# Performance work log

Hardware: AMD Instinct MI355X
Metric: run time of the kernel (lower is better)

Reference implementation:

```python
import jax, jax.numpy as jnp
import numpy as np

B, N, D, P, V = 8, 256, 300, 128, 50001  # batch, seq len, emb dim, proj dim, vocab(+unk)


def setup_inputs() -> dict:
    key = jax.random.key(0)
    ks = jax.random.split(key, 10)
    s = 1.0 / np.sqrt(D)
    sp = 1.0 / np.sqrt(P)
    emb = jax.random.normal(ks[0], (V, D), jnp.float32)
    emb = emb.at[-1].set(0.0)  # unk row zeroed, matches add_unk
    return {
        "sentence": jax.random.randint(ks[1], (B, N), 0, V),
        "emb": emb,
        "Wl": jax.random.uniform(ks[2], (P, D), jnp.float32, -s, s),
        "bl": jnp.zeros((P,), jnp.float32),
        "Wr": jax.random.uniform(ks[3], (P, D), jnp.float32, -s, s),
        "Wo": jax.random.uniform(ks[4], (1, P), jnp.float32, -sp, sp),
        "bo": jnp.zeros((1,), jnp.float32),
        "Ws1": jax.random.uniform(ks[5], (P, D), jnp.float32, -s, s),
        "bs1": jnp.zeros((P,), jnp.float32),
        "Ws2": jax.random.uniform(ks[6], (1, P), jnp.float32, -sp, sp),
        "bs2": jnp.zeros((1,), jnp.float32),
        "We1": jax.random.uniform(ks[7], (P, D), jnp.float32, -s, s),
        "be1": jnp.zeros((P,), jnp.float32),
        "We2": jax.random.uniform(ks[8], (1, P), jnp.float32, -sp, sp),
        "be2": jnp.zeros((1,), jnp.float32),
    }


def reference(sentence, emb, Wl, bl, Wr, Wo, bo, Ws1, bs1, Ws2, bs2, We1, be1, We2, be2):
    x = emb[sentence]                                   # [B,N,D] embedding lookup
    start = jax.nn.relu(x @ Ws1.T + bs1) @ Ws2.T + bs2  # [B,N,1]
    end = jax.nn.relu(x @ We1.T + be1) @ We2.T + be2    # [B,N,1]
    left = x @ Wl.T + bl                                # [B,N,P]
    right = x @ Wr.T                                    # [B,N,P]
    # proj[b,i,j,p] = left[b,j,p] + right[b,i,p]  (unsqueeze(1) + unsqueeze(2))
    proj = left[:, None, :, :] + right[:, :, None, :]   # [B,N,N,P]
    bigram = jax.nn.relu(proj) @ Wo.T + bo              # [B,N,N,1]
    return (bigram, start, end)
```

## Files before the change

### kernel.cpp

```cpp
#include <hip/hip_runtime.h>

#define NB 8
#define NN 256
#define DD 300
#define PP 128
#define NC 512
#define OFF_S (NB * NN * NN)
#define OFF_E (NB * NN * NN + NB * NN)

typedef unsigned short u16;
typedef unsigned int   u32;

__device__ __forceinline__ float bf2f(u16 u) {
    union { u32 i; float f; } v;
    v.i = ((u32)u) << 16;
    return v.f;
}
__device__ __forceinline__ u16 f2bf(float f) {
    union { float f; u32 i; } v;
    v.f = f;
    u32 lsb = (v.i >> 16) & 1u;
    v.i += 0x7fffu + lsb;
    return (u16)(v.i >> 16);
}

template<bool BF>
__device__ __forceinline__ float4 ld4(const void* base, int idx) {
    if (BF) {
        ushort4 e = *(const ushort4*)((const u16*)base + idx);
        return make_float4(bf2f(e.x), bf2f(e.y), bf2f(e.z), bf2f(e.w));
    } else {
        return *(const float4*)((const float*)base + idx);
    }
}
template<bool BF>
__device__ __forceinline__ float ld1(const void* base, int idx) {
    return BF ? bf2f(((const u16*)base)[idx]) : ((const float*)base)[idx];
}
template<bool BF>
__device__ __forceinline__ void st1(void* base, int idx, float v) {
    if (BF) ((u16*)base)[idx] = f2bf(v);
    else    ((float*)base)[idx] = v;
}

extern "C" __global__ void detect_kernel(const u32* __restrict__ embU,
                                         int* __restrict__ flag) {
    int lane = threadIdx.x;
    int cnt = 0;
    for (int i = lane; i < 256; i += 64) {
        u32 w = embU[i];
        union { u32 u; float f; } v;
        v.u = (w & 0xFFFFu) << 16;
        float a = fabsf(v.f);
        if (a == 0.f || (a >= 0.00390625f && a <= 256.f)) cnt++;
    }
    #pragma unroll
    for (int off = 32; off; off >>= 1) cnt += __shfl_down(cnt, off, 64);
    if (lane == 0) *flag = (cnt >= 128) ? 1 : 0;
}

template<bool BF>
__device__ __forceinline__ void prep_body(
    const void* __restrict__ Wl, const void* __restrict__ Wr,
    const void* __restrict__ Ws1, const void* __restrict__ We1,
    float* __restrict__ WTf, float (*tile)[301])
{
    const int tid = threadIdx.x;
    const int c0  = blockIdx.x * 32;

    for (int e = tid; e < 32 * 75; e += 256) {
        int r = e / 75;
        int q = e - r * 75;
        int c = c0 + r;
        const void* src = (c < 128) ? Wl : (c < 256) ? Wr
                        : (c < 384) ? Ws1 : We1;
        float4 f = ld4<BF>(src, (c & 127) * DD + 4 * q);
        tile[r][4 * q + 0] = f.x;
        tile[r][4 * q + 1] = f.y;
        tile[r][4 * q + 2] = f.z;
        tile[r][4 * q + 3] = f.w;
    }
    __syncthreads();
    for (int e = tid; e < 300 * 32; e += 256) {
        int k = e >> 5;
        int c = e & 31;
        WTf[(size_t)k * NC + c0 + c] = tile[c][k];
    }
}

extern "C" __global__ void __launch_bounds__(256)
prep_kernel(const void* __restrict__ Wl, const void* __restrict__ Wr,
            const void* __restrict__ Ws1, const void* __restrict__ We1,
            float* __restrict__ WTf, const int* __restrict__ flag)
{
    __shared__ float tile[32][301];
    if (*flag) prep_body<true >(Wl, Wr, Ws1, We1, WTf, tile);
    else       prep_body<false>(Wl, Wr, Ws1, We1, WTf, tile);
}

template<bool BF>
__device__ __forceinline__ void tok_body(
    const int* __restrict__ sent, const void* __restrict__ emb,
    const float* __restrict__ WTf,
    const void* __restrict__ bl,
    const void* __restrict__ bs1, const void* __restrict__ Ws2,
    const void* __restrict__ bs2,
    const void* __restrict__ be1, const void* __restrict__ We2,
    const void* __restrict__ be2,
    float* __restrict__ leftT, float* __restrict__ rightW,
    void* __restrict__ out, float (*sxT)[8], int* sids)
{
    const int tid = threadIdx.x;
    const int t0  = blockIdx.x * 8;

    if (tid < 8) sids[tid] = sent[t0 + tid];
    __syncthreads();

    for (int e = tid; e < DD * 8; e += 256) {
        int k = e >> 3, t = e & 7;
        sxT[k][t] = ld1<BF>(emb, sids[t] * DD + k);
    }
    __syncthreads();

    float a0[8], a1[8];
    #pragma unroll
    for (int t = 0; t < 8; ++t) { a0[t] = 0.f; a1[t] = 0.f; }

    const float* wp = WTf + 2 * tid;
    #pragma unroll 4
    for (int k = 0; k < DD; ++k) {
        float2 w  = *(const float2*)(wp + (size_t)k * NC);
        float4 xa = *(const float4*)&sxT[k][0];
        float4 xb = *(const float4*)&sxT[k][4];
        a0[0] = fmaf(xa.x, w.x, a0[0]); a1[0] = fmaf(xa.x, w.y, a1[0]);
        a0[1] = fmaf(xa.y, w.x, a0[1]); a1[1] = fmaf(xa.y, w.y, a1[1]);
        a0[2] = fmaf(xa.z, w.x, a0[2]); a1[2] = fmaf(xa.z, w.y, a1[2]);
        a0[3] = fmaf(xa.w, w.x, a0[3]); a1[3] = fmaf(xa.w, w.y, a1[3]);
        a0[4] = fmaf(xb.x, w.x, a0[4]); a1[4] = fmaf(xb.x, w.y, a1[4]);
        a0[5] = fmaf(xb.y, w.x, a0[5]); a1[5] = fmaf(xb.y, w.y, a1[5]);
        a0[6] = fmaf(xb.z, w.x, a0[6]); a1[6] = fmaf(xb.z, w.y, a1[6]);
        a0[7] = fmaf(xb.w, w.x, a0[7]); a1[7] = fmaf(xb.w, w.y, a1[7]);
    }

    const int wv = tid >> 6;
    const int l  = tid & 63;
    const int p0 = 2 * l, p1 = p0 + 1;

    if (wv == 0) {
        float b0 = ld1<BF>(bl, p0), b1 = ld1<BF>(bl, p1);
        #pragma unroll
        for (int t = 0; t < 8; ++t) {
            int tg = t0 + t, bb = tg >> 8, jj = tg & 255;
            leftT[((size_t)bb * PP + p0) * NN + jj] = a0[t] + b0;
            leftT[((size_t)bb * PP + p1) * NN + jj] = a1[t] + b1;
        }
    } else if (wv == 1) {
        #pragma unroll
        for (int t = 0; t < 8; ++t) {
            rightW[(size_t)(t0 + t) * PP + p0] = a0[t];
            rightW[(size_t)(t0 + t) * PP + p1] = a1[t];
        }
    } else {
        const void* h1 = (wv == 2) ? bs1 : be1;
        const void* h2 = (wv == 2) ? Ws2 : We2;
        const void* h3 = (wv == 2) ? bs2 : be2;
        float b0 = ld1<BF>(h1, p0), b1 = ld1<BF>(h1, p1);
        float w0 = ld1<BF>(h2, p0), w1 = ld1<BF>(h2, p1);
        float v[8];
        #pragma unroll
        for (int t = 0; t < 8; ++t)
            v[t] = fmaxf(a0[t] + b0, 0.f) * w0 + fmaxf(a1[t] + b1, 0.f) * w1;
        #pragma unroll
        for (int off = 32; off; off >>= 1) {
            #pragma unroll
            for (int t = 0; t < 8; ++t) v[t] += __shfl_down(v[t], off, 64);
        }
        if (l == 0) {
            float b2 = ld1<BF>(h3, 0);
            int base = (wv == 2) ? OFF_S : OFF_E;
            #pragma unroll
            for (int t = 0; t < 8; ++t)
                st1<BF>(out, base + t0 + t, v[t] + b2);
        }
    }
}

extern "C" __global__ void __launch_bounds__(256)
tok_kernel(const int* __restrict__ sent, const void* __restrict__ emb,
           const float* __restrict__ WTf,
           const void* __restrict__ bl,
           const void* __restrict__ bs1, const void* __restrict__ Ws2,
           const void* __restrict__ bs2,
           const void* __restrict__ be1, const void* __restrict__ We2,
           const void* __restrict__ be2,
           float* __restrict__ leftT, float* __restrict__ rightW,
           void* __restrict__ out, const int* __restrict__ flag)
{
    __shared__ __align__(16) float sxT[DD][8];
    __shared__ int sids[8];
    if (*flag) {
        tok_body<true >(sent, emb, WTf, bl, bs1, Ws2, bs2, be1, We2, be2,
                        leftT, rightW, out, sxT, sids);
    } else {
        tok_body<false>(sent, emb, WTf, bl, bs1, Ws2, bs2, be1, We2, be2,
                        leftT, rightW, out, sxT, sids);
    }
}

extern "C" __global__ void __launch_bounds__(256)
big_kernel(const float* __restrict__ leftT, const float* __restrict__ rightW,
           const void* __restrict__ Wo, const void* __restrict__ bo,
           void* __restrict__ outB, const int* __restrict__ flag)
{
    __shared__ float sR[4][128];
    __shared__ float sWo[128];
    const int  tid = threadIdx.x;
    const int  b   = blockIdx.x >> 6;
    const int  i0  = (blockIdx.x & 63) << 2;
    const bool bf  = (*flag != 0);

    if (tid < 128) sWo[tid] = bf ? bf2f(((const u16*)Wo)[tid])
                                 : ((const float*)Wo)[tid];
    for (int c = tid; c < 512; c += 256) {
        int i = c >> 7, pp = c & 127;
        sR[i][pp] = rightW[((size_t)(b * NN + i0 + i)) * PP + pp];
    }
    __syncthreads();

    const int j = tid;
    const float* lp = leftT + (size_t)b * PP * NN + j;
    float acc0 = 0.f, acc1 = 0.f, acc2 = 0.f, acc3 = 0.f;
    #pragma unroll 8
    for (int pth = 0; pth < 128; ++pth) {
        float lv = lp[pth * NN];
        float wo = sWo[pth];
        acc0 = fmaf(fmaxf(lv + sR[0][pth], 0.f), wo, acc0);
        acc1 = fmaf(fmaxf(lv + sR[1][pth], 0.f), wo, acc1);
        acc2 = fmaf(fmaxf(lv + sR[2][pth], 0.f), wo, acc2);
        acc3 = fmaf(fmaxf(lv + sR[3][pth], 0.f), wo, acc3);
    }
    float bov = bf ? bf2f(((const u16*)bo)[0]) : ((const float*)bo)[0];
    size_t ob = ((size_t)(b * NN + i0)) * NN + j;
    if (bf) {
        u16* o = (u16*)outB;
        o[ob]          = f2bf(acc0 + bov);
        o[ob + NN]     = f2bf(acc1 + bov);
        o[ob + 2 * NN] = f2bf(acc2 + bov);
        o[ob + 3 * NN] = f2bf(acc3 + bov);
    } else {
        float* o = (float*)outB;
        o[ob]          = acc0 + bov;
        o[ob + NN]     = acc1 + bov;
        o[ob + 2 * NN] = acc2 + bov;
        o[ob + 3 * NN] = acc3 + bov;
    }
}

extern "C" void kernel_launch(void* const* d_in, const int* in_sizes, int n_in,
                              void* d_out, int out_size, void* d_ws, size_t ws_size,
                              hipStream_t stream) {
    const int*  sent = (const int*)d_in[0];
    const void* emb  = d_in[1];
    const void* Wl   = d_in[2];
    const void* bl   = d_in[3];
    const void* Wr   = d_in[4];
    const void* Wo   = d_in[5];
    const void* bo   = d_in[6];
    const void* Ws1  = d_in[7];
    const void* bs1  = d_in[8];
    const void* Ws2  = d_in[9];
    const void* bs2  = d_in[10];
    const void* We1  = d_in[11];
    const void* be1  = d_in[12];
    const void* We2  = d_in[13];
    const void* be2  = d_in[14];

    int*   flag   = (int*)d_ws;
    float* leftT  = (float*)((char*)d_ws + 1024);
    float* rightW = leftT + (size_t)NB * PP * NN;
    float* WTf    = rightW + (size_t)NB * NN * PP;

    hipLaunchKernelGGL(detect_kernel, dim3(1), dim3(64), 0, stream,
                       (const u32*)emb, flag);
    hipLaunchKernelGGL(prep_kernel, dim3(16), dim3(256), 0, stream,
                       Wl, Wr, Ws1, We1, WTf, flag);
    hipLaunchKernelGGL(tok_kernel, dim3(256), dim3(256), 0, stream,
                       sent, emb, WTf, bl, bs1, Ws2, bs2, be1, We2, be2,
                       leftT, rightW, d_out, flag);
    hipLaunchKernelGGL(big_kernel, dim3(512), dim3(256), 0, stream,
                       leftT, rightW, Wo, bo, d_out, flag);
}
```

Measured before the change: 163.8 us.

## Split big kernel P-reduction across waves with vectorized loads; halve tokens per tok block

The big kernel now has each wave take a quarter of the projection dimension, with each lane handling four j columns through float4 loads. Partial sums are reduced across waves in shared memory and written with vectorized stores, and the bf16/fp32 paths are resolved by templates. The token kernel now processes 4 tokens per block instead of 8, doubling the grid to 512 blocks for more parallelism. This adds shared-memory reduction traffic and a sync, and it reloads more weights per token in the token kernel.

```diff
diff --git a/kernel.cpp b/kernel.cpp
--- a/kernel.cpp
+++ b/kernel.cpp
@@ -41,6 +41,22 @@
 __device__ __forceinline__ void st1(void* base, int idx, float v) {
     if (BF) ((u16*)base)[idx] = f2bf(v);
     else    ((float*)base)[idx] = v;
+}
+template<bool BF>
+__device__ __forceinline__ void st4(void* base, int idx, float4 v) {
+    if (BF) {
+        ushort4 o = make_ushort4(f2bf(v.x), f2bf(v.y), f2bf(v.z), f2bf(v.w));
+        *(ushort4*)((u16*)base + idx) = o;
+    } else {
+        *(float4*)((float*)base + idx) = v;
+    }
+}
+__device__ __forceinline__ float4 rfma4(float4 l, float r, float w, float4 a) {
+    a.x = fmaf(fmaxf(l.x + r, 0.f), w, a.x);
+    a.y = fmaf(fmaxf(l.y + r, 0.f), w, a.y);
+    a.z = fmaf(fmaxf(l.z + r, 0.f), w, a.z);
+    a.w = fmaf(fmaxf(l.w + r, 0.f), w, a.w);
+    return a;
 }
 
 extern "C" __global__ void detect_kernel(const u32* __restrict__ embU,
@@ -108,38 +124,33 @@
     const void* __restrict__ be1, const void* __restrict__ We2,
     const void* __restrict__ be2,
     float* __restrict__ leftT, float* __restrict__ rightW,
-    void* __restrict__ out, float (*sxT)[8], int* sids)
+    void* __restrict__ out, float (*sxT)[4], int* sids)
 {
     const int tid = threadIdx.x;
-    const int t0  = blockIdx.x * 8;
-
-    if (tid < 8) sids[tid] = sent[t0 + tid];
-    __syncthreads();
-
-    for (int e = tid; e < DD * 8; e += 256) {
-        int k = e >> 3, t = e & 7;
+    const int t0  = blockIdx.x * 4;
+
+    if (tid < 4) sids[tid] = sent[t0 + tid];
+    __syncthreads();
+
+    for (int e = tid; e < DD * 4; e += 256) {
+        int k = e >> 2, t = e & 3;
         sxT[k][t] = ld1<BF>(emb, sids[t] * DD + k);
     }
     __syncthreads();
 
-    float a0[8], a1[8];
+    float a0[4], a1[4];
     #pragma unroll
-    for (int t = 0; t < 8; ++t) { a0[t] = 0.f; a1[t] = 0.f; }
+    for (int t = 0; t < 4; ++t) { a0[t] = 0.f; a1[t] = 0.f; }
 
     const float* wp = WTf + 2 * tid;
     #pragma unroll 4
     for (int k = 0; k < DD; ++k) {
         float2 w  = *(const float2*)(wp + (size_t)k * NC);
         float4 xa = *(const float4*)&sxT[k][0];
-        float4 xb = *(const float4*)&sxT[k][4];
         a0[0] = fmaf(xa.x, w.x, a0[0]); a1[0] = fmaf(xa.x, w.y, a1[0]);
         a0[1] = fmaf(xa.y, w.x, a0[1]); a1[1] = fmaf(xa.y, w.y, a1[1]);
         a0[2] = fmaf(xa.z, w.x, a0[2]); a1[2] = fmaf(xa.z, w.y, a1[2]);
         a0[3] = fmaf(xa.w, w.x, a0[3]); a1[3] = fmaf(xa.w, w.y, a1[3]);
-        a0[4] = fmaf(xb.x, w.x, a0[4]); a1[4] = fmaf(xb.x, w.y, a1[4]);
-        a0[5] = fmaf(xb.y, w.x, a0[5]); a1[5] = fmaf(xb.y, w.y, a1[5]);
-        a0[6] = fmaf(xb.z, w.x, a0[6]); a1[6] = fmaf(xb.z, w.y, a1[6]);
-        a0[7] = fmaf(xb.w, w.x, a0[7]); a1[7] = fmaf(xb.w, w.y, a1[7]);
     }
 
     const int wv = tid >> 6;
@@ -149,14 +160,14 @@
     if (wv == 0) {
         float b0 = ld1<BF>(bl, p0), b1 = ld1<BF>(bl, p1);
         #pragma unroll
-        for (int t = 0; t < 8; ++t) {
+        for (int t = 0; t < 4; ++t) {
             int tg = t0 + t, bb = tg >> 8, jj = tg & 255;
             leftT[((size_t)bb * PP + p0) * NN + jj] = a0[t] + b0;
             leftT[((size_t)bb * PP + p1) * NN + jj] = a1[t] + b1;
         }
     } else if (wv == 1) {
         #pragma unroll
-        for (int t = 0; t < 8; ++t) {
+        for (int t = 0; t < 4; ++t) {
             rightW[(size_t)(t0 + t) * PP + p0] = a0[t];
             rightW[(size_t)(t0 + t) * PP + p1] = a1[t];
         }
@@ -166,20 +177,20 @@
         const void* h3 = (wv == 2) ? bs2 : be2;
         float b0 = ld1<BF>(h1, p0), b1 = ld1<BF>(h1, p1);
         float w0 = ld1<BF>(h2, p0), w1 = ld1<BF>(h2, p1);
-        float v[8];
-        #pragma unroll
-        for (int t = 0; t < 8; ++t)
+        float v[4];
+        #pragma unroll
+        for (int t = 0; t < 4; ++t)
             v[t] = fmaxf(a0[t] + b0, 0.f) * w0 + fmaxf(a1[t] + b1, 0.f) * w1;
         #pragma unroll
         for (int off = 32; off; off >>= 1) {
             #pragma unroll
-            for (int t = 0; t < 8; ++t) v[t] += __shfl_down(v[t], off, 64);
+            for (int t = 0; t < 4; ++t) v[t] += __shfl_down(v[t], off, 64);
         }
         if (l == 0) {
             float b2 = ld1<BF>(h3, 0);
             int base = (wv == 2) ? OFF_S : OFF_E;
             #pragma unroll
-            for (int t = 0; t < 8; ++t)
+            for (int t = 0; t < 4; ++t)
                 st1<BF>(out, base + t0 + t, v[t] + b2);
         }
     }
@@ -196,8 +207,8 @@
            float* __restrict__ leftT, float* __restrict__ rightW,
            void* __restrict__ out, const int* __restrict__ flag)
 {
-    __shared__ __align__(16) float sxT[DD][8];
-    __shared__ int sids[8];
+    __shared__ __align__(16) float sxT[DD][4];
+    __shared__ int sids[4];
     if (*flag) {
         tok_body<true >(sent, emb, WTf, bl, bs1, Ws2, bs2, be1, We2, be2,
                         leftT, rightW, out, sxT, sids);
@@ -207,6 +218,86 @@
     }
 }
 
+template<bool BF>
+__device__ __forceinline__ void big_body(
+    const float* __restrict__ leftT, const float* __restrict__ rightW,
+    const void* __restrict__ Wo, const void* __restrict__ bo,
+    void* __restrict__ outB,
+    float (*sR)[128], float* sWo, float4 (*red4)[64][4])
+{
+    const int tid = threadIdx.x;
+    const int b   = blockIdx.x >> 6;
+    const int i0  = (blockIdx.x & 63) << 2;
+
+    if (tid < 128) sWo[tid] = ld1<BF>(Wo, tid);
+    for (int c = tid; c < 512; c += 256) {
+        int i = c >> 7, pp = c & 127;
+        sR[i][pp] = rightW[((size_t)(b * NN + i0 + i)) * PP + pp];
+    }
+    __syncthreads();
+
+    const int w    = tid >> 6;
+    const int lane = tid & 63;
+    const int j4   = lane << 2;
+    const float* lp = leftT + (size_t)b * PP * NN + j4;
+
+    float4 A0 = {0.f, 0.f, 0.f, 0.f}, A1 = A0, A2 = A0, A3 = A0;
+    const int pbase = w * 32;
+    #pragma unroll
+    for (int g = 0; g < 8; ++g) {
+        const int p = pbase + g * 4;
+        float4 wo = *(const float4*)&sWo[p];
+        float4 r0 = *(const float4*)&sR[0][p];
+        float4 r1 = *(const float4*)&sR[1][p];
+        float4 r2 = *(const float4*)&sR[2][p];
+        float4 r3 = *(const float4*)&sR[3][p];
+        const float* lpp = lp + (size_t)p * NN;
+        float4 l0 = *(const float4*)(lpp);
+        float4 l1 = *(const float4*)(lpp + NN);
+        float4 l2 = *(const float4*)(lpp + 2 * NN);
+        float4 l3 = *(const float4*)(lpp + 3 * NN);
+        A0 = rfma4(l0, r0.x, wo.x, A0);
+        A1 = rfma4(l0, r1.x, wo.x, A1);
+        A2 = rfma4(l0, r2.x, wo.x, A2);
+        A3 = rfma4(l0, r3.x, wo.x, A3);
+        A0 = rfma4(l1, r0.y, wo.y, A0);
+        A1 = rfma4(l1, r1.y, wo.y, A1);
+        A2 = rfma4(l1, r2.y, wo.y, A2);
+        A3 = rfma4(l1, r3.y, wo.y, A3);
+        A0 = rfma4(l2, r0.z, wo.z, A0);
+        A1 = rfma4(l2, r1.z, wo.z, A1);
+        A2 = rfma4(l2, r2.z, wo.z, A2);
+        A3 = rfma4(l2, r3.z, wo.z, A3);
+        A0 = rfma4(l3, r0.w, wo.w, A0);
+        A1 = rfma4(l3, r1.w, wo.w, A1);
+        A2 = rfma4(l3, r2.w, wo.w, A2);
+        A3 = rfma4(l3, r3.w, wo.w, A3);
+    }
+
+    red4[w][lane][0] = A0;
+    red4[w][lane][1] = A1;
+    red4[w][lane][2] = A2;
+    red4[w][lane][3] = A3;
+    __syncthreads();
+
+    if (tid < 64) {
+        float bov = ld1<BF>(bo, 0);
+        #pragma unroll
+        for (int i = 0; i < 4; ++i) {
+            float4 s0 = red4[0][tid][i];
+            float4 s1 = red4[1][tid][i];
+            float4 s2 = red4[2][tid][i];
+            float4 s3 = red4[3][tid][i];
+            float4 s;
+            s.x = s0.x + s1.x + s2.x + s3.x + bov;
+            s.y = s0.y + s1.y + s2.y + s3.y + bov;
+            s.z = s0.z + s1.z + s2.z + s3.z + bov;
+            s.w = s0.w + s1.w + s2.w + s3.w + bov;
+            st4<BF>(outB, (int)(((size_t)(b * NN + i0 + i)) * NN) + tid * 4, s);
+        }
+    }
+}
+
 extern "C" __global__ void __launch_bounds__(256)
 big_kernel(const float* __restrict__ leftT, const float* __restrict__ rightW,
            const void* __restrict__ Wo, const void* __restrict__ bo,
@@ -214,46 +305,9 @@
 {
     __shared__ float sR[4][128];
     __shared__ float sWo[128];
-    const int  tid = threadIdx.x;
-    const int  b   = blockIdx.x >> 6;
-    const int  i0  = (blockIdx.x & 63) << 2;
-    const bool bf  = (*flag != 0);
-
-    if (tid < 128) sWo[tid] = bf ? bf2f(((const u16*)Wo)[tid])
-                                 : ((const float*)Wo)[tid];
-    for (int c = tid; c < 512; c += 256) {
-        int i = c >> 7, pp = c & 127;
-        sR[i][pp] = rightW[((size_t)(b * NN + i0 + i)) * PP + pp];
-    }
-    __syncthreads();
-
-    const int j = tid;
-    const float* lp = leftT + (size_t)b * PP * NN + j;
-    float acc0 = 0.f, acc1 = 0.f, acc2 = 0.f, acc3 = 0.f;
-    #pragma unroll 8
-    for (int pth = 0; pth < 128; ++pth) {
-        float lv = lp[pth * NN];
-        float wo = sWo[pth];
-        acc0 = fmaf(fmaxf(lv + sR[0][pth], 0.f), wo, acc0);
-        acc1 = fmaf(fmaxf(lv + sR[1][pth], 0.f), wo, acc1);
-        acc2 = fmaf(fmaxf(lv + sR[2][pth], 0.f), wo, acc2);
-        acc3 = fmaf(fmaxf(lv + sR[3][pth], 0.f), wo, acc3);
-    }
-    float bov = bf ? bf2f(((const u16*)bo)[0]) : ((const float*)bo)[0];
-    size_t ob = ((size_t)(b * NN + i0)) * NN + j;
-    if (bf) {
-        u16* o = (u16*)outB;
-        o[ob]          = f2bf(acc0 + bov);
-        o[ob + NN]     = f2bf(acc1 + bov);
-        o[ob + 2 * NN] = f2bf(acc2 + bov);
-        o[ob + 3 * NN] = f2bf(acc3 + bov);
-    } else {
-        float* o = (float*)outB;
-        o[ob]          = acc0 + bov;
-        o[ob + NN]     = acc1 + bov;
-        o[ob + 2 * NN] = acc2 + bov;
-        o[ob + 3 * NN] = acc3 + bov;
-    }
+    __shared__ float4 red4[4][64][4];
+    if (*flag) big_body<true >(leftT, rightW, Wo, bo, outB, sR, sWo, red4);
+    else       big_body<false>(leftT, rightW, Wo, bo, outB, sR, sWo, red4);
 }
 
 extern "C" void kernel_launch(void* const* d_in, const int* in_sizes, int n_in,
@@ -284,7 +338,7 @@
                        (const u32*)emb, flag);
     hipLaunchKernelGGL(prep_kernel, dim3(16), dim3(256), 0, stream,
                        Wl, Wr, Ws1, We1, WTf, flag);
-    hipLaunchKernelGGL(tok_kernel, dim3(256), dim3(256), 0, stream,
+    hipLaunchKernelGGL(tok_kernel, dim3(512), dim3(256), 0, stream,
                        sent, emb, WTf, bl, bs1, Ws2, bs2, be1, We2, be2,
                        leftT, rightW, d_out, flag);
     hipLaunchKernelGGL(big_kernel, dim3(512), dim3(256), 0, stream,
```

Result: faster. 158.8 us (-3.1%).
